# Kernel optimization log

Hardware: AMD Instinct MI355X
Metric: run time of the kernel (lower is better)

Reference implementation:

```python
import jax, jax.numpy as jnp
import numpy as np

N = 100000   # num nodes
E = 1600000  # num edges
D = 256      # input feature dim (dataset.num_features)


def setup_inputs() -> dict:
    key = jax.random.key(0)
    ks = jax.random.split(key, 10)

    def w(k, fan_in, fan_out):
        return jax.random.normal(k, (fan_in, fan_out), jnp.float32) / jnp.sqrt(fan_in)

    return {
        "x": jax.random.normal(ks[0], (N, D), jnp.float32),
        "edge_index": jax.random.randint(ks[1], (2, E), 0, N, jnp.int32),
        "W1": w(ks[2], D, 128),   "b1": jnp.zeros((128,), jnp.float32),
        "W2": w(ks[3], 128, 128), "b2": jnp.zeros((128,), jnp.float32),
        "W3": w(ks[4], 128, 64),  "b3": jnp.zeros((64,), jnp.float32),
        "W4": w(ks[5], 64, 32),   "b4": jnp.zeros((32,), jnp.float32),
    }


def _gcn_norm(edge_index, n):
    # GCNConv default: add self-loops, symmetric deg^-1/2 normalization
    loops = jnp.arange(n, dtype=edge_index.dtype)
    src = jnp.concatenate([edge_index[0], loops])
    dst = jnp.concatenate([edge_index[1], loops])
    deg = jax.ops.segment_sum(jnp.ones_like(dst, jnp.float32), dst, num_segments=n)
    dinv = jnp.where(deg > 0, jax.lax.rsqrt(deg), 0.0)
    norm = dinv[src] * dinv[dst]  # [E+N]
    return src, dst, norm


def _gcn_layer(x, W, b, src, dst, norm, n):
    h = x @ W                          # [N, out]
    msg = h[src] * norm[:, None]       # gather + scale: [E+N, out]
    agg = jax.ops.segment_sum(msg, dst, num_segments=n)  # scatter-add
    return agg + b


def reference(x, edge_index, W1, b1, W2, b2, W3, b3, W4, b4):
    n = x.shape[0]
    src, dst, norm = _gcn_norm(edge_index, n)
    h = jax.nn.relu(_gcn_layer(x, W1, b1, src, dst, norm, n))
    h = jax.nn.relu(_gcn_layer(h, W2, b2, src, dst, norm, n))
    h = jax.nn.relu(_gcn_layer(h, W3, b3, src, dst, norm, n))
    return _gcn_layer(h, W4, b4, src, dst, norm, n)  # encode() output z: [N, 32]
```

## Files before the change

### kernel.cpp

```cpp
#include <hip/hip_runtime.h>

#define CDIV(a,b) (((a)+(b)-1)/(b))
#define BUK_SHIFT 10
#define EPB 4096

typedef float f32x4 __attribute__((ext_vector_type(4)));
typedef short short8 __attribute__((ext_vector_type(8)));
typedef _Float16 h16x8 __attribute__((ext_vector_type(8)));


__device__ inline unsigned short rne_bf16(float f) {
    unsigned int u = __builtin_bit_cast(unsigned int, f);
    u += 0x7FFFu + ((u >> 16) & 1u);
    return (unsigned short)(u >> 16);
}

struct BF16Pair { short hi, lo; };

__device__ inline BF16Pair split_bf16(float f) {
    unsigned short h = rne_bf16(f);
    float fh = __builtin_bit_cast(float, (unsigned int)h << 16);
    BF16Pair p;
    p.hi = (short)h;
    p.lo = (short)rne_bf16(f - fh);
    return p;
}


__global__ void dinv_kernel(const int* __restrict__ cnt, float* dinv, int n) {
    int i = blockIdx.x * blockDim.x + threadIdx.x;
    if (i < n) dinv[i] = rsqrtf((float)cnt[i] + 1.0f);
}

__global__ __launch_bounds__(512) void scan_block_kernel(const int* __restrict__ cnt,
                                                         int* rp, int* aux, int N) {
    __shared__ int s[512];
    int t = threadIdx.x;
    int i = blockIdx.x * 512 + t;
    int v = (i < N) ? cnt[i] : 0;
    s[t] = v;
    __syncthreads();
    for (int off = 1; off < 512; off <<= 1) {
        int x = (t >= off) ? s[t - off] : 0;
        __syncthreads();
        s[t] += x;
        __syncthreads();
    }
    if (i < N) rp[i] = s[t] - v;
    if (t == 511) aux[blockIdx.x] = s[511];
}

__global__ __launch_bounds__(256) void scan_aux_kernel(int* aux, int nb) {
    __shared__ int s[256];
    int t = threadIdx.x;
    int v = (t < nb) ? aux[t] : 0;
    s[t] = v;
    __syncthreads();
    for (int off = 1; off < 256; off <<= 1) {
        int x = (t >= off) ? s[t - off] : 0;
        __syncthreads();
        s[t] += x;
        __syncthreads();
    }
    if (t < nb) aux[t] = s[t] - v;
}

__global__ void scan_add_kernel(int* rp, const int* __restrict__ aux, int N, int E) {
    int i = blockIdx.x * blockDim.x + threadIdx.x;
    if (i < N) rp[i] += aux[i >> 9];
    if (i == N) rp[N] = E;
}

__global__ void copy_int_kernel(const int* __restrict__ rp, int* fill, int n) {
    int i = blockIdx.x * blockDim.x + threadIdx.x;
    if (i < n) fill[i] = rp[i];
}


__global__ __launch_bounds__(256) void bkt_hist_kernel(const int* __restrict__ dst,
                                                       int* __restrict__ hcnt,
                                                       int E, int nbuk, int nblk) {
    __shared__ int lh[128];
    int t = threadIdx.x;
    for (int i = t; i < nbuk; i += 256) lh[i] = 0;
    __syncthreads();
    int base = blockIdx.x * EPB;
    int end = min(base + EPB, E);
    for (int e = base + t; e < end; e += 256)
        atomicAdd(&lh[dst[e] >> BUK_SHIFT], 1);
    __syncthreads();
    for (int i = t; i < nbuk; i += 256) hcnt[i * nblk + blockIdx.x] = lh[i];
}

__global__ __launch_bounds__(1024) void scan_flat_kernel(int* a, int n) {
    __shared__ int s[1024];
    int t = threadIdx.x;
    int per = (n + 1023) / 1024;
    int start = t * per, end = min(start + per, n);
    int sum = 0;
    for (int i = start; i < end; ++i) sum += a[i];
    s[t] = sum;
    __syncthreads();
    for (int off = 1; off < 1024; off <<= 1) {
        int x = (t >= off) ? s[t - off] : 0;
        __syncthreads();
        s[t] += x;
        __syncthreads();
    }
    int run = s[t] - sum;
    for (int i = start; i < end; ++i) { int v = a[i]; a[i] = run; run += v; }
}

__global__ __launch_bounds__(256) void bkt_scatter_kernel(const int* __restrict__ src,
                                                          const int* __restrict__ dst,
                                                          const int* __restrict__ obk,
                                                          unsigned long long* __restrict__ ebuf,
                                                          int E, int nbuk, int nblk) {
    __shared__ int cur[128];
    int t = threadIdx.x;
    for (int i = t; i < nbuk; i += 256) cur[i] = obk[i * nblk + blockIdx.x];
    __syncthreads();
    int base = blockIdx.x * EPB;
    int end = min(base + EPB, E);
    for (int e = base + t; e < end; e += 256) {
        int d = dst[e], s = src[e];
        int b = d >> BUK_SHIFT;
        int pos = atomicAdd(&cur[b], 1);
        ebuf[pos] = ((unsigned long long)(unsigned)d << 32) | (unsigned)s;
    }
}

__global__ __launch_bounds__(1024) void node_hist_kernel(const unsigned long long* __restrict__ ebuf,
                                                         const int* __restrict__ hcnt,
                                                         int* __restrict__ cnt,
                                                         int E, int N, int nbuk, int nblk) {
    __shared__ int lh[1024];
    const int b = blockIdx.x;
    const int t = threadIdx.x;
    lh[t] = 0;
    __syncthreads();
    const int st = hcnt[b * nblk];
    const int en = (b + 1 < nbuk) ? hcnt[(b + 1) * nblk] : E;
    for (int e = st + t; e < en; e += 1024) {
        int d = (int)(unsigned)(ebuf[e] >> 32);
        atomicAdd(&lh[d & 1023], 1);
    }
    __syncthreads();
    int node = (b << BUK_SHIFT) + t;
    if (node < N) cnt[node] = lh[t];
}

__global__ void fill_csr_kernel(const unsigned long long* __restrict__ ebuf,
                                int* fill, int* __restrict__ col, int E) {
    int e = blockIdx.x * blockDim.x + threadIdx.x;
    if (e >= E) return;
    unsigned long long r = ebuf[e];
    int s = (int)(unsigned)(r & 0xFFFFFFFFull);
    int d = (int)(unsigned)(r >> 32);
    int pos = atomicAdd(&fill[d], 1);
    col[pos] = s;
}


template<int K, int F>
__global__ void wprep_kernel(const float* __restrict__ W, short* __restrict__ whi,
                             short* __restrict__ wlo) {
    constexpr int CB = F / 16;
    int idx = blockIdx.x * 256 + threadIdx.x;
    if (idx >= K * F) return;
    int e = idx & 7;
    int lane = (idx >> 3) & 63;
    int fc = idx >> 9;
    int kb = fc / CB, cb = fc % CB;
    int k = kb * 32 + (lane >> 4) * 8 + e;
    int colv = cb * 16 + (lane & 15);
    BF16Pair p = split_bf16(W[k * F + colv]);
    whi[idx] = p.hi;
    wlo[idx] = p.lo;
}


template<int K, int F, typename AT>
__global__ __launch_bounds__(256) void mfma_gemm(const AT* __restrict__ A,
                                                 const short* __restrict__ Whi,
                                                 const short* __restrict__ Wlo,
                                                 const float* __restrict__ dinv,
                                                 _Float16* __restrict__ H, int N) {
    constexpr int CB = F / 16;
    constexpr int KB = K / 32;
    constexpr int HCH = CB * 64;
    constexpr int CHUNKS = HCH * 2;
    constexpr int CPT = (CHUNKS + 255) / 256;

    __shared__ __align__(16) short Bs[2][CB * 1024];

    const int tid = threadIdx.x;
    const int wid = tid >> 6, lane = tid & 63;
    const int rowf = lane & 15;
    const int kgrp = lane >> 4;
    const long long row0 = (long long)blockIdx.x * 64 + wid * 16;

    f32x4 acc[CB] = {};
    short8 breg[CPT];
    float fvaC[8], fvaN[8];

    auto stage_issue = [&](int kb) {
#pragma unroll
        for (int i = 0; i < CPT; ++i) {
            int c = tid + i * 256;
            if (CHUNKS < 256 && c >= CHUNKS) continue;
            const short* p = (c < HCH) ? (Whi + (size_t)kb * (CB * 512) + (size_t)c * 8)
                                       : (Wlo + (size_t)kb * (CB * 512) + (size_t)(c - HCH) * 8);
            breg[i] = *(const short8*)p;
        }
    };
    auto stage_write = [&](int b) {
#pragma unroll
        for (int i = 0; i < CPT; ++i) {
            int c = tid + i * 256;
            if (CHUNKS < 256 && c >= CHUNKS) continue;
            *(short8*)&Bs[b][(size_t)c * 8] = breg[i];
        }
    };
    auto a_load = [&](float (&dst)[8], int kb) {
        long long r = row0 + rowf;
        if (r < N) {
            const AT* ap = A + (size_t)r * K + kb * 32 + kgrp * 8;
            if constexpr (sizeof(AT) == 4) {
                float4 f0 = ((const float4*)ap)[0];
                float4 f1 = ((const float4*)ap)[1];
                dst[0]=f0.x; dst[1]=f0.y; dst[2]=f0.z; dst[3]=f0.w;
                dst[4]=f1.x; dst[5]=f1.y; dst[6]=f1.z; dst[7]=f1.w;
            } else {
                h16x8 hv = *(const h16x8*)ap;
#pragma unroll
                for (int j = 0; j < 8; ++j) dst[j] = (float)hv[j];
            }
        } else {
#pragma unroll
            for (int j = 0; j < 8; ++j) dst[j] = 0.f;
        }
    };

    stage_issue(0);
    a_load(fvaC, 0);

    for (int kb = 0; kb < KB; ++kb) {
        const int b = kb & 1;
        stage_write(b);
        if (kb + 1 < KB) stage_issue(kb + 1);
        asm volatile("s_waitcnt lgkmcnt(0)" ::: "memory");
        __builtin_amdgcn_s_barrier();
        __builtin_amdgcn_sched_barrier(0);
        if (kb + 1 < KB) a_load(fvaN, kb + 1);

        short8 ahi, alo;
#pragma unroll
        for (int j = 0; j < 8; ++j) {
            BF16Pair p = split_bf16(fvaC[j]);
            ahi[j] = p.hi;
            alo[j] = p.lo;
        }
#pragma unroll
        for (int cb = 0; cb < CB; ++cb) {
            short8 bhi = *(const short8*)&Bs[b][((size_t)cb * 64 + lane) * 8];
            short8 blo = *(const short8*)&Bs[b][CB * 512 + ((size_t)cb * 64 + lane) * 8];
            acc[cb] = __builtin_amdgcn_mfma_f32_16x16x32_bf16(ahi, bhi, acc[cb], 0, 0, 0);
            acc[cb] = __builtin_amdgcn_mfma_f32_16x16x32_bf16(alo, bhi, acc[cb], 0, 0, 0);
            acc[cb] = __builtin_amdgcn_mfma_f32_16x16x32_bf16(ahi, blo, acc[cb], 0, 0, 0);
        }
#pragma unroll
        for (int j = 0; j < 8; ++j) fvaC[j] = fvaN[j];
    }

    const int rsub = (lane >> 4) * 4;
    long long rbase = row0 + rsub;
    float dv[4];
#pragma unroll
    for (int j = 0; j < 4; ++j) dv[j] = (rbase + j < N) ? dinv[rbase + j] : 0.f;
#pragma unroll
    for (int cb = 0; cb < CB; ++cb) {
        int colv = cb * 16 + rowf;
#pragma unroll
        for (int j = 0; j < 4; ++j) {
            long long r = rbase + j;
            if (r < N) H[(size_t)r * F + colv] = (_Float16)(acc[cb][j] * dv[j]);
        }
    }
}


template<int F, bool RELU, typename OutT>
__global__ __launch_bounds__(256) void agg_kernel(const _Float16* __restrict__ hs,
                                                  const int* __restrict__ rp,
                                                  const int* __restrict__ col,
                                                  const float* __restrict__ dinv,
                                                  const float* __restrict__ bias,
                                                  OutT* __restrict__ out, int N) {
    constexpr int LPN = F / 8;
    constexpr int NPB = 256 / LPN;
    const int tid = threadIdx.x;
    const int lane = tid % LPN;
    const int node = blockIdx.x * NPB + tid / LPN;
    if (node >= N) return;

    const int f0 = lane * 8;
    const _Float16* hbase = hs + f0;

    float acc[8];
    {
        h16x8 sv = *(const h16x8*)(hbase + (size_t)node * F);
#pragma unroll
        for (int v = 0; v < 8; ++v) acc[v] = (float)sv[v];
    }

    int e = rp[node];
    const int e1 = rp[node + 1];
    for (; e + 4 <= e1; e += 4) {
        int s0 = col[e], s1 = col[e + 1], s2 = col[e + 2], s3 = col[e + 3];
        h16x8 v0 = *(const h16x8*)(hbase + (size_t)s0 * F);
        h16x8 v1 = *(const h16x8*)(hbase + (size_t)s1 * F);
        h16x8 v2 = *(const h16x8*)(hbase + (size_t)s2 * F);
        h16x8 v3 = *(const h16x8*)(hbase + (size_t)s3 * F);
#pragma unroll
        for (int v = 0; v < 8; ++v)
            acc[v] += ((float)v0[v] + (float)v1[v]) + ((float)v2[v] + (float)v3[v]);
    }
    for (; e < e1; ++e) {
        h16x8 v0 = *(const h16x8*)(hbase + (size_t)col[e] * F);
#pragma unroll
        for (int v = 0; v < 8; ++v) acc[v] += (float)v0[v];
    }

    const float self = dinv[node];
    OutT* op = out + (size_t)node * F + f0;
    const float* bp = bias + f0;
#pragma unroll
    for (int v = 0; v < 8; ++v) {
        float r = fmaf(acc[v], self, bp[v]);
        if (RELU) r = fmaxf(r, 0.f);
        op[v] = (OutT)r;
    }
}


extern "C" void kernel_launch(void* const* d_in, const int* in_sizes, int n_in,
                              void* d_out, int out_size, void* d_ws, size_t ws_size,
                              hipStream_t stream) {
    const float* x  = (const float*)d_in[0];
    const int*   ei = (const int*)d_in[1];
    const float* W1 = (const float*)d_in[2];
    const float* b1 = (const float*)d_in[3];
    const float* W2 = (const float*)d_in[4];
    const float* b2 = (const float*)d_in[5];
    const float* W3 = (const float*)d_in[6];
    const float* b3 = (const float*)d_in[7];
    const float* W4 = (const float*)d_in[8];
    const float* b4 = (const float*)d_in[9];

    const int N = in_sizes[0] / 256;
    const int E = in_sizes[1] / 2;
    const int* src = ei;
    const int* dst = ei + E;

    const int NB   = CDIV(N, 512);
    const int nbuk = ((N - 1) >> BUK_SHIFT) + 1;
    const int nblk = CDIV(E, EPB);

    char* base = (char*)d_ws;
    size_t o = 0;
    auto alloc = [&](size_t bytes) { char* p = base + o; o += (bytes + 255) & ~(size_t)255; return p; };
    int*   cnt  = (int*)  alloc(sizeof(int) * N);
    int*   rp   = (int*)  alloc(sizeof(int) * (N + 1));
    int*   aux  = (int*)  alloc(sizeof(int) * 256);
    float* dinv = (float*)alloc(sizeof(float) * N);
    int*   col  = (int*)  alloc(sizeof(int) * E);
    int*   hcnt = (int*)  alloc(sizeof(int) * (size_t)nbuk * nblk);
    unsigned long long* ebuf = (unsigned long long*)alloc(sizeof(unsigned long long) * E);
    short* w1h  = (short*)alloc(sizeof(short) * 256 * 128);
    short* w1l  = (short*)alloc(sizeof(short) * 256 * 128);
    short* w2h  = (short*)alloc(sizeof(short) * 128 * 128);
    short* w2l  = (short*)alloc(sizeof(short) * 128 * 128);
    short* w3h  = (short*)alloc(sizeof(short) * 128 * 64);
    short* w3l  = (short*)alloc(sizeof(short) * 128 * 64);
    short* w4h  = (short*)alloc(sizeof(short) * 64 * 32);
    short* w4l  = (short*)alloc(sizeof(short) * 64 * 32);
    _Float16* hsbuf = (_Float16*)alloc(sizeof(_Float16) * (size_t)N * 128);
    _Float16* zsbuf = (_Float16*)alloc(sizeof(_Float16) * (size_t)N * 128);
    float* out  = (float*)d_out;

    wprep_kernel<256, 128><<<CDIV(256 * 128, 256), 256, 0, stream>>>(W1, w1h, w1l);
    wprep_kernel<128, 128><<<CDIV(128 * 128, 256), 256, 0, stream>>>(W2, w2h, w2l);
    wprep_kernel<128, 64><<<CDIV(128 * 64, 256), 256, 0, stream>>>(W3, w3h, w3l);
    wprep_kernel<64, 32><<<CDIV(64 * 32, 256), 256, 0, stream>>>(W4, w4h, w4l);

    bkt_hist_kernel<<<nblk, 256, 0, stream>>>(dst, hcnt, E, nbuk, nblk);
    scan_flat_kernel<<<1, 1024, 0, stream>>>(hcnt, nbuk * nblk);
    bkt_scatter_kernel<<<nblk, 256, 0, stream>>>(src, dst, hcnt, ebuf, E, nbuk, nblk);

    node_hist_kernel<<<nbuk, 1024, 0, stream>>>(ebuf, hcnt, cnt, E, N, nbuk, nblk);
    dinv_kernel<<<CDIV(N, 256), 256, 0, stream>>>(cnt, dinv, N);
    scan_block_kernel<<<NB, 512, 0, stream>>>(cnt, rp, aux, N);
    scan_aux_kernel<<<1, 256, 0, stream>>>(aux, NB);
    scan_add_kernel<<<CDIV(N + 1, 256), 256, 0, stream>>>(rp, aux, N, E);
    copy_int_kernel<<<CDIV(N, 256), 256, 0, stream>>>(rp, cnt, N);
    fill_csr_kernel<<<CDIV(E, 256), 256, 0, stream>>>(ebuf, cnt, col, E);

    const int GG = CDIV(N, 64);

    mfma_gemm<256, 128, float><<<GG, 256, 0, stream>>>(x, w1h, w1l, dinv, hsbuf, N);
    agg_kernel<128, true, _Float16><<<CDIV(N, 16), 256, 0, stream>>>(hsbuf, rp, col, dinv, b1, zsbuf, N);

    mfma_gemm<128, 128, _Float16><<<GG, 256, 0, stream>>>(zsbuf, w2h, w2l, dinv, hsbuf, N);
    agg_kernel<128, true, _Float16><<<CDIV(N, 16), 256, 0, stream>>>(hsbuf, rp, col, dinv, b2, zsbuf, N);

    mfma_gemm<128, 64, _Float16><<<GG, 256, 0, stream>>>(zsbuf, w3h, w3l, dinv, hsbuf, N);
    agg_kernel<64, true, _Float16><<<CDIV(N, 32), 256, 0, stream>>>(hsbuf, rp, col, dinv, b3, zsbuf, N);

    mfma_gemm<64, 32, _Float16><<<GG, 256, 0, stream>>>(zsbuf, w4h, w4l, dinv, hsbuf, N);
    agg_kernel<32, false, float><<<CDIV(N, 64), 256, 0, stream>>>(hsbuf, rp, col, dinv, b4, out, N);
}
```

Measured before the change: 411.9 us.

## Fuse per-bucket degree count, scan, dinv and CSR fill into one kernel

Replaces the node histogram, dinv, three-stage global scan, copy and global-atomic CSR fill kernels with one per-bucket kernel. Because edges are already bucketed by destination, each 1024-node bucket computes degrees, a local exclusive scan offset by the bucket start, dinv, and fills col using shared-memory atomics. This removes six launches, the global atomics on the fill array, and intermediate arrays. In exchange, only about 98 blocks of 1024 threads do the CSR fill, so parallelism is lower, and each bucket re-reads ebuf.

```diff
diff --git a/kernel.cpp b/kernel.cpp
--- a/kernel.cpp
+++ b/kernel.cpp
@@ -24,56 +24,6 @@
     p.hi = (short)h;
     p.lo = (short)rne_bf16(f - fh);
     return p;
-}
-
-
-__global__ void dinv_kernel(const int* __restrict__ cnt, float* dinv, int n) {
-    int i = blockIdx.x * blockDim.x + threadIdx.x;
-    if (i < n) dinv[i] = rsqrtf((float)cnt[i] + 1.0f);
-}
-
-__global__ __launch_bounds__(512) void scan_block_kernel(const int* __restrict__ cnt,
-                                                         int* rp, int* aux, int N) {
-    __shared__ int s[512];
-    int t = threadIdx.x;
-    int i = blockIdx.x * 512 + t;
-    int v = (i < N) ? cnt[i] : 0;
-    s[t] = v;
-    __syncthreads();
-    for (int off = 1; off < 512; off <<= 1) {
-        int x = (t >= off) ? s[t - off] : 0;
-        __syncthreads();
-        s[t] += x;
-        __syncthreads();
-    }
-    if (i < N) rp[i] = s[t] - v;
-    if (t == 511) aux[blockIdx.x] = s[511];
-}
-
-__global__ __launch_bounds__(256) void scan_aux_kernel(int* aux, int nb) {
-    __shared__ int s[256];
-    int t = threadIdx.x;
-    int v = (t < nb) ? aux[t] : 0;
-    s[t] = v;
-    __syncthreads();
-    for (int off = 1; off < 256; off <<= 1) {
-        int x = (t >= off) ? s[t - off] : 0;
-        __syncthreads();
-        s[t] += x;
-        __syncthreads();
-    }
-    if (t < nb) aux[t] = s[t] - v;
-}
-
-__global__ void scan_add_kernel(int* rp, const int* __restrict__ aux, int N, int E) {
-    int i = blockIdx.x * blockDim.x + threadIdx.x;
-    if (i < N) rp[i] += aux[i >> 9];
-    if (i == N) rp[N] = E;
-}
-
-__global__ void copy_int_kernel(const int* __restrict__ rp, int* fill, int n) {
-    int i = blockIdx.x * blockDim.x + threadIdx.x;
-    if (i < n) fill[i] = rp[i];
 }
 
 
@@ -130,35 +80,48 @@
     }
 }
 
-__global__ __launch_bounds__(1024) void node_hist_kernel(const unsigned long long* __restrict__ ebuf,
-                                                         const int* __restrict__ hcnt,
-                                                         int* __restrict__ cnt,
-                                                         int E, int N, int nbuk, int nblk) {
+__global__ __launch_bounds__(1024) void bucket_csr_kernel(const unsigned long long* __restrict__ ebuf,
+                                                          const int* __restrict__ hcnt,
+                                                          int* __restrict__ rp,
+                                                          float* __restrict__ dinv,
+                                                          int* __restrict__ col,
+                                                          int E, int N, int nbuk, int nblk) {
     __shared__ int lh[1024];
+    __shared__ int lsc[1024];
     const int b = blockIdx.x;
     const int t = threadIdx.x;
     lh[t] = 0;
     __syncthreads();
     const int st = hcnt[b * nblk];
     const int en = (b + 1 < nbuk) ? hcnt[(b + 1) * nblk] : E;
+    for (int e = st + t; e < en; e += 1024)
+        atomicAdd(&lh[((int)(unsigned)(ebuf[e] >> 32)) & 1023], 1);
+    __syncthreads();
+    const int deg = lh[t];
+    lsc[t] = deg;
+    __syncthreads();
+    for (int off = 1; off < 1024; off <<= 1) {
+        int x = (t >= off) ? lsc[t - off] : 0;
+        __syncthreads();
+        lsc[t] += x;
+        __syncthreads();
+    }
+    const int excl = lsc[t] - deg;
+    const int node = (b << BUK_SHIFT) + t;
+    if (node < N) {
+        rp[node] = st + excl;
+        dinv[node] = rsqrtf((float)deg + 1.0f);
+    }
+    if (b == 0 && t == 0) rp[N] = E;
+    __syncthreads();
+    lh[t] = st + excl;
+    __syncthreads();
     for (int e = st + t; e < en; e += 1024) {
-        int d = (int)(unsigned)(ebuf[e] >> 32);
-        atomicAdd(&lh[d & 1023], 1);
-    }
-    __syncthreads();
-    int node = (b << BUK_SHIFT) + t;
-    if (node < N) cnt[node] = lh[t];
-}
-
-__global__ void fill_csr_kernel(const unsigned long long* __restrict__ ebuf,
-                                int* fill, int* __restrict__ col, int E) {
-    int e = blockIdx.x * blockDim.x + threadIdx.x;
-    if (e >= E) return;
-    unsigned long long r = ebuf[e];
-    int s = (int)(unsigned)(r & 0xFFFFFFFFull);
-    int d = (int)(unsigned)(r >> 32);
-    int pos = atomicAdd(&fill[d], 1);
-    col[pos] = s;
+        unsigned long long r = ebuf[e];
+        int d = (int)(unsigned)(r >> 32);
+        int pos = atomicAdd(&lh[d & 1023], 1);
+        col[pos] = (int)(unsigned)(r & 0xFFFFFFFFull);
+    }
 }
 
 
@@ -363,16 +326,13 @@
     const int* src = ei;
     const int* dst = ei + E;
 
-    const int NB   = CDIV(N, 512);
     const int nbuk = ((N - 1) >> BUK_SHIFT) + 1;
     const int nblk = CDIV(E, EPB);
 
     char* base = (char*)d_ws;
     size_t o = 0;
     auto alloc = [&](size_t bytes) { char* p = base + o; o += (bytes + 255) & ~(size_t)255; return p; };
-    int*   cnt  = (int*)  alloc(sizeof(int) * N);
     int*   rp   = (int*)  alloc(sizeof(int) * (N + 1));
-    int*   aux  = (int*)  alloc(sizeof(int) * 256);
     float* dinv = (float*)alloc(sizeof(float) * N);
     int*   col  = (int*)  alloc(sizeof(int) * E);
     int*   hcnt = (int*)  alloc(sizeof(int) * (size_t)nbuk * nblk);
@@ -398,13 +358,7 @@
     scan_flat_kernel<<<1, 1024, 0, stream>>>(hcnt, nbuk * nblk);
     bkt_scatter_kernel<<<nblk, 256, 0, stream>>>(src, dst, hcnt, ebuf, E, nbuk, nblk);
 
-    node_hist_kernel<<<nbuk, 1024, 0, stream>>>(ebuf, hcnt, cnt, E, N, nbuk, nblk);
-    dinv_kernel<<<CDIV(N, 256), 256, 0, stream>>>(cnt, dinv, N);
-    scan_block_kernel<<<NB, 512, 0, stream>>>(cnt, rp, aux, N);
-    scan_aux_kernel<<<1, 256, 0, stream>>>(aux, NB);
-    scan_add_kernel<<<CDIV(N + 1, 256), 256, 0, stream>>>(rp, aux, N, E);
-    copy_int_kernel<<<CDIV(N, 256), 256, 0, stream>>>(rp, cnt, N);
-    fill_csr_kernel<<<CDIV(E, 256), 256, 0, stream>>>(ebuf, cnt, col, E);
+    bucket_csr_kernel<<<nbuk, 1024, 0, stream>>>(ebuf, hcnt, rp, dinv, col, E, N, nbuk, nblk);
 
     const int GG = CDIV(N, 64);
 
```

Result: faster. 367.2 us (-10.8%).
